# Kernel tuning notes

Hardware: AMD Instinct MI355X
Metric: run time of the kernel (lower is better)

Reference implementation:

```python
import jax, jax.numpy as jnp
import numpy as np

OUTDIM, INPUTDIM, DEGREE = 64, 512, 8


def setup_inputs() -> dict:
    key = jax.random.key(0)
    k1, k2 = jax.random.split(key)
    x = jax.random.normal(k1, (16, 4096, INPUTDIM), dtype=jnp.float32)
    # torch.randn(outdim, inputdim, degree) / (sqrt(inputdim)*sqrt(degree))
    coeffs = jax.random.normal(k2, (OUTDIM, INPUTDIM, DEGREE), dtype=jnp.float32)
    coeffs = coeffs / (np.sqrt(INPUTDIM) * np.sqrt(DEGREE))
    bias = jnp.zeros((1, OUTDIM), dtype=jnp.float32)
    return {"x": x, "coeffs": coeffs, "bias": bias}


def _legendre_basis(xn, degree):
    # Iterative (memoized) Legendre recurrence; xn in [-1, 1], shape [N, I].
    Ps = [jnp.ones_like(xn)]
    if degree > 1:
        Ps.append(xn)
    for n in range(2, degree):
        Ps.append(((2.0 * n - 1.0) * xn * Ps[-1] - (n - 1.0) * Ps[-2]) / n)
    return jnp.stack(Ps, axis=-1)  # [N, I, D]


def reference(x, coeffs, bias):
    outdim, inputdim, degree = coeffs.shape
    outshape = x.shape[:-1] + (outdim,)
    x2 = x.reshape(-1, inputdim)                      # [N, I]
    xmin, xmax = x2.min(), x2.max()                   # global min-max normalize
    xn = 2.0 * (x2 - xmin) / (xmax - xmin) - 1.0
    P = _legendre_basis(xn, degree)                   # [N, I, D]
    y = jnp.einsum("nid,oid->no", P, coeffs)          # contract input & degree
    y = y + bias                                      # [N, O]
    return y.reshape(outshape)
```

## Files before the change

kernel.cpp:

```cpp
#include <hip/hip_runtime.h>
#include <math.h>


typedef __bf16 bf16x8 __attribute__((ext_vector_type(8)));
typedef float f32x4 __attribute__((ext_vector_type(4)));

__global__ __launch_bounds__(256) void k_minmax_partial(
    const float4* __restrict__ x4, int n4, float* __restrict__ pmn, float* __restrict__ pmx)
{
  float mn = 3.4e38f, mx = -3.4e38f;
  int stride = gridDim.x * 256;
  for (int i = blockIdx.x * 256 + threadIdx.x; i < n4; i += stride) {
    float4 v = x4[i];
    mn = fminf(mn, fminf(fminf(v.x, v.y), fminf(v.z, v.w)));
    mx = fmaxf(mx, fmaxf(fmaxf(v.x, v.y), fmaxf(v.z, v.w)));
  }
  #pragma unroll
  for (int off = 32; off > 0; off >>= 1) {
    mn = fminf(mn, __shfl_down(mn, off));
    mx = fmaxf(mx, __shfl_down(mx, off));
  }
  __shared__ float smn[4], smx[4];
  int w = threadIdx.x >> 6;
  if ((threadIdx.x & 63) == 0) { smn[w] = mn; smx[w] = mx; }
  __syncthreads();
  if (threadIdx.x == 0) {
    pmn[blockIdx.x] = fminf(fminf(smn[0], smn[1]), fminf(smn[2], smn[3]));
    pmx[blockIdx.x] = fmaxf(fmaxf(smx[0], smx[1]), fmaxf(smx[2], smx[3]));
  }
}

__global__ __launch_bounds__(256) void k_prep_final(
    const float* __restrict__ coeffs, bf16x8* __restrict__ Bws,
    const float* __restrict__ pmn, const float* __restrict__ pmx, int nb,
    float* __restrict__ so, float* __restrict__ y, const float* __restrict__ bias,
    int doB)
{
  int b = blockIdx.x;
  if (b < 128) {
    if (!doB) return;
    int t = b * 256 + threadIdx.x;
    int lane = t & 63;
    int tile = t >> 6;
    int ct = tile & 3;
    int kt = tile >> 2;
    int i = kt * 4 + (lane >> 4);
    int o = ct * 16 + (lane & 15);
    const float4* cp = (const float4*)(coeffs + ((size_t)o * 512 + i) * 8);
    float4 c0 = cp[0], c1 = cp[1];
    bf16x8 v;
    v[0] = (__bf16)(c0.x);
    v[1] = (__bf16)(c0.y);
    v[2] = (__bf16)(c0.z * 1.5f);
    v[3] = (__bf16)(c0.w * 2.5f);
    v[4] = (__bf16)(c1.x * 4.375f);
    v[5] = (__bf16)(c1.y * 7.875f);
    v[6] = (__bf16)(c1.z * 14.4375f);
    v[7] = (__bf16)(c1.w * 26.8125f);
    Bws[(size_t)(kt * 4 + ct) * 64 + lane] = v;
  } else if (b == 128) {
    float mn = 3.4e38f, mx = -3.4e38f;
    for (int i = threadIdx.x; i < nb; i += 256) {
      mn = fminf(mn, pmn[i]);
      mx = fmaxf(mx, pmx[i]);
    }
    #pragma unroll
    for (int off = 32; off > 0; off >>= 1) {
      mn = fminf(mn, __shfl_down(mn, off));
      mx = fmaxf(mx, __shfl_down(mx, off));
    }
    __shared__ float smn[4], smx[4];
    int w = threadIdx.x >> 6;
    if ((threadIdx.x & 63) == 0) { smn[w] = mn; smx[w] = mx; }
    __syncthreads();
    if (threadIdx.x == 0) {
      mn = fminf(fminf(smn[0], smn[1]), fminf(smn[2], smn[3]));
      mx = fmaxf(fmaxf(smx[0], smx[1]), fmaxf(smx[2], smx[3]));
      float r = mx - mn;
      so[0] = 2.0f / r;
      so[1] = -2.0f * mn / r - 1.0f;
    }
  } else {
    int base = (b - 129) * 1024;
    const float4* b4 = (const float4*)bias;
    float4* y4 = (float4*)y;
    #pragma unroll
    for (int r = 0; r < 4; ++r) {
      int j = base + r * 256 + threadIdx.x;
      y4[j] = b4[j & 15];
    }
  }
}

__global__ __launch_bounds__(256, 4) void k_main(
    const float* __restrict__ x, const bf16x8* __restrict__ Bws,
    const float* __restrict__ so, float* __restrict__ y)
{
  __shared__ __align__(16) float4 smem[2048];

  const float s = so[0], off = so[1];
  const int t    = threadIdx.x;
  const int lane = t & 63;
  const int w    = t >> 6;
  const int m    = lane & 15;
  const int quad = lane >> 4;
  const int bx   = blockIdx.x;
  const int qK   = bx & 3;
  const size_t rowbase = ((size_t)(bx >> 2)) * 128 + (size_t)w * 32;
  const int kb0 = qK * 32;

  const float* xq0 = x + (rowbase +      m) * 512 + (size_t)kb0 * 4 + quad;
  const float* xq1 = x + (rowbase + 16 + m) * 512 + (size_t)kb0 * 4 + quad;

  const float4* bsrc = (const float4*)((const char*)Bws + (size_t)kb0 * 4096);

  f32x4 acc[2][4];
  #pragma unroll
  for (int f = 0; f < 2; ++f)
    #pragma unroll
    for (int ct = 0; ct < 4; ++ct) acc[f][ct] = (f32x4){0.f, 0.f, 0.f, 0.f};

  const float C2 = 0.33333334f, C3 = 0.26666668f, C4 = 0.25714287f;
  const float C5 = 0.25396827f, C6 = 0.25252524f, C7 = 0.25174826f;

  float xr[4][2];
  xr[0][0] = xq0[0];  xr[0][1] = xq1[0];
  xr[1][0] = xq0[4];  xr[1][1] = xq1[4];

  const bf16x8* bw = (const bf16x8*)smem;

  for (int wi = 0; wi < 4; ++wi) {
    __syncthreads();
    {
      const float4* g = bsrc + (size_t)wi * 2048;
      float4 a0 = g[t], a1 = g[t + 256], a2 = g[t + 512], a3 = g[t + 768];
      smem[t] = a0; smem[t + 256] = a1; smem[t + 512] = a2; smem[t + 768] = a3;
      float4 b0 = g[t + 1024], b1 = g[t + 1280], b2 = g[t + 1536], b3 = g[t + 1792];
      smem[t + 1024] = b0; smem[t + 1280] = b1; smem[t + 1536] = b2; smem[t + 1792] = b3;
    }
    __syncthreads();

    bf16x8 Bq[2][4];
    #pragma unroll
    for (int ct = 0; ct < 4; ++ct) Bq[0][ct] = bw[ct * 64 + lane];

    #pragma unroll
    for (int kl = 0; kl < 8; ++kl) {
      const int l = wi * 8 + kl;

      if (kl < 7) {
        #pragma unroll
        for (int ct = 0; ct < 4; ++ct)
          Bq[(kl + 1) & 1][ct] = bw[((kl + 1) * 4 + ct) * 64 + lane];
      }
      {
        const int lp = (l + 2 < 32) ? (l + 2) : 31;
        xr[(kl + 2) & 3][0] = xq0[lp * 4];
        xr[(kl + 2) & 3][1] = xq1[lp * 4];
      }

      bf16x8 a[2];
      #pragma unroll
      for (int f = 0; f < 2; ++f) {
        float xn = fmaf(xr[kl & 3][f], s, off);
        float s2 = fmaf(xn, xn, -C2);
        float s3 = (s2 - C3) * xn;
        float s4 = fmaf(xn, s3, -(C4 * s2));
        float s5 = fmaf(xn, s4, -(C5 * s3));
        float s6 = fmaf(xn, s5, -(C6 * s4));
        float s7 = fmaf(xn, s6, -(C7 * s5));
        bf16x8 av;
        av[0] = (__bf16)1.0f; av[1] = (__bf16)xn; av[2] = (__bf16)s2; av[3] = (__bf16)s3;
        av[4] = (__bf16)s4;   av[5] = (__bf16)s5; av[6] = (__bf16)s6; av[7] = (__bf16)s7;
        a[f] = av;
      }

      #pragma unroll
      for (int f = 0; f < 2; ++f)
        #pragma unroll
        for (int ct = 0; ct < 4; ++ct)
          acc[f][ct] = __builtin_amdgcn_mfma_f32_16x16x32_bf16(a[f], Bq[kl & 1][ct], acc[f][ct], 0, 0, 0);
    }
  }

  #pragma unroll
  for (int f = 0; f < 2; ++f) {
    float* yp = y + (rowbase + f * 16 + quad * 4) * 64 + m;
    #pragma unroll
    for (int ct = 0; ct < 4; ++ct)
      #pragma unroll
      for (int r = 0; r < 4; ++r)
        atomicAdd(yp + r * 64 + ct * 16, acc[f][ct][r]);
  }
}

__global__ __launch_bounds__(256) void k_main_simple(
    const float* __restrict__ x, const float* __restrict__ coeffs,
    const float* __restrict__ bias, const float* __restrict__ so, float* __restrict__ y)
{
  const float s = so[0], off = so[1];
  const int lane = threadIdx.x & 63;
  const int w    = threadIdx.x >> 6;
  const int m    = lane & 15;
  const int quad = lane >> 4;
  const int rowA = blockIdx.x * 64 + w * 16 + m;
  const float* xp = x + (size_t)rowA * 512 + quad;

  f32x4 acc0 = {0.f,0.f,0.f,0.f}, acc1 = acc0, acc2 = acc0, acc3 = acc0;
  const float c3a = 5.f/3.f, c3b = 2.f/3.f, c6a = 11.f/6.f, c6b = 5.f/6.f, c7a = 13.f/7.f, c7b = 6.f/7.f;

  for (int kt = 0; kt < 128; ++kt) {
    float xv = xp[kt * 4];
    int i = kt * 4 + quad;
    bf16x8 b[4];
    #pragma unroll
    for (int ct = 0; ct < 4; ++ct) {
      const float* cp = coeffs + ((size_t)(ct * 16 + m) * 512 + i) * 8;
      #pragma unroll
      for (int j = 0; j < 8; ++j) b[ct][j] = (__bf16)cp[j];
    }
    float xn = fmaf(xv, s, off);
    float p2 = fmaf(1.5f * xn, xn, -0.5f);
    float p3 = fmaf(c3a * xn, p2, -(c3b * xn));
    float p4 = fmaf(1.75f * xn, p3, -(0.75f * p2));
    float p5 = fmaf(1.8f * xn, p4, -(0.8f * p3));
    float p6 = fmaf(c6a * xn, p5, -(c6b * p4));
    float p7 = fmaf(c7a * xn, p6, -(c7b * p5));
    bf16x8 a;
    a[0] = (__bf16)1.0f; a[1] = (__bf16)xn; a[2] = (__bf16)p2; a[3] = (__bf16)p3;
    a[4] = (__bf16)p4;   a[5] = (__bf16)p5; a[6] = (__bf16)p6; a[7] = (__bf16)p7;
    acc0 = __builtin_amdgcn_mfma_f32_16x16x32_bf16(a, b[0], acc0, 0, 0, 0);
    acc1 = __builtin_amdgcn_mfma_f32_16x16x32_bf16(a, b[1], acc1, 0, 0, 0);
    acc2 = __builtin_amdgcn_mfma_f32_16x16x32_bf16(a, b[2], acc2, 0, 0, 0);
    acc3 = __builtin_amdgcn_mfma_f32_16x16x32_bf16(a, b[3], acc3, 0, 0, 0);
  }
  float b0v = bias[m], b1v = bias[16+m], b2v = bias[32+m], b3v = bias[48+m];
  float* yp = y + ((size_t)(blockIdx.x * 64 + w * 16 + quad * 4)) * 64 + m;
  #pragma unroll
  for (int r = 0; r < 4; ++r) {
    yp[r*64+ 0] = acc0[r] + b0v;
    yp[r*64+16] = acc1[r] + b1v;
    yp[r*64+32] = acc2[r] + b2v;
    yp[r*64+48] = acc3[r] + b3v;
  }
}

extern "C" void kernel_launch(void* const* d_in, const int* in_sizes, int n_in,
                              void* d_out, int out_size, void* d_ws, size_t ws_size,
                              hipStream_t stream)
{
  const float* x      = (const float*)d_in[0];
  const float* coeffs = (const float*)d_in[1];
  const float* bias   = (const float*)d_in[2];
  float* y = (float*)d_out;

  long nx = (long)in_sizes[0];
  int  N  = (int)(nx / 512);
  int  n4 = (int)(nx / 4);

  float*  so  = (float*)d_ws;
  float*  pmn = (float*)d_ws + 16;
  float*  pmx = pmn + 4096;
  bf16x8* Bws = (bf16x8*)((char*)d_ws + 65536);

  bool pre = ws_size >= (size_t)(65536 + 4096 * 64 * 2 + 4096);

  const int MMB = 4096;
  k_minmax_partial<<<MMB, 256, 0, stream>>>((const float4*)x, n4, pmn, pmx);
  k_prep_final<<<1153, 256, 0, stream>>>(coeffs, Bws, pmn, pmx, MMB, so, y, bias, pre ? 1 : 0);

  if (pre) {
    k_main<<<(N / 128) * 4, 256, 0, stream>>>(x, Bws, so, y);
  } else {
    k_main_simple<<<N / 64, 256, 0, stream>>>(x, coeffs, bias, so, y);
  }
}
```

Measured before the change: 284.3 us.

## Stage coalesced x tiles and Legendre basis in LDS with register-prefetched pipeline

Each thread now loads contiguous float4 chunks of x instead of strided scalar loads, and evaluates the Legendre basis once per element. The bf16 basis vectors go into a padded LDS buffer (stride 17) that the MFMA fragments then read. B and x for the next slice are prefetched into registers while the current slice is multiplied. The goal is to remove uncoalesced global reads of x and redundant basis work. The cost is more LDS (about 50KB), occupancy lowered to 3 blocks per CU, and an extra barrier per iteration.

After: 266.7 us. -6.2%, faster.

```diff
diff --git a/kernel.cpp b/kernel.cpp
--- a/kernel.cpp
+++ b/kernel.cpp
@@ -4,6 +4,8 @@
 
 typedef __bf16 bf16x8 __attribute__((ext_vector_type(8)));
 typedef float f32x4 __attribute__((ext_vector_type(4)));
+
+#define ASTRIDE 17
 
 __global__ __launch_bounds__(256) void k_minmax_partial(
     const float4* __restrict__ x4, int n4, float* __restrict__ pmn, float* __restrict__ pmx)
@@ -92,11 +94,14 @@
   }
 }
 
-__global__ __launch_bounds__(256, 4) void k_main(
+__global__ __launch_bounds__(256, 3) void k_main(
     const float* __restrict__ x, const bf16x8* __restrict__ Bws,
     const float* __restrict__ so, float* __restrict__ y)
 {
-  __shared__ __align__(16) float4 smem[2048];
+  __shared__ __align__(16) char smem[51200];
+  bf16x8* As = (bf16x8*)smem;
+  bf16x8* Bs = (bf16x8*)(smem + 34816);
+  float4* Bs4 = (float4*)Bs;
 
   const float s = so[0], off = so[1];
   const int t    = threadIdx.x;
@@ -106,13 +111,18 @@
   const int quad = lane >> 4;
   const int bx   = blockIdx.x;
   const int qK   = bx & 3;
-  const size_t rowbase = ((size_t)(bx >> 2)) * 128 + (size_t)w * 32;
-  const int kb0 = qK * 32;
-
-  const float* xq0 = x + (rowbase +      m) * 512 + (size_t)kb0 * 4 + quad;
-  const float* xq1 = x + (rowbase + 16 + m) * 512 + (size_t)kb0 * 4 + quad;
-
-  const float4* bsrc = (const float4*)((const char*)Bws + (size_t)kb0 * 4096);
+  const size_t rowbase = ((size_t)(bx >> 2)) * 128;
+
+  const int srow  = t >> 1;
+  const int shalf = t & 1;
+  const float* xg = x + (rowbase + srow) * 512 + qK * 128 + shalf * 8;
+  const int awbase = srow * ASTRIDE + shalf * 8;
+
+  const float4* bsrc = (const float4*)(Bws + (size_t)qK * 32 * 256);
+
+  int arb[2];
+  #pragma unroll
+  for (int f = 0; f < 2; ++f) arb[f] = (w * 32 + f * 16 + m) * ASTRIDE + quad;
 
   f32x4 acc[2][4];
   #pragma unroll
@@ -123,69 +133,63 @@
   const float C2 = 0.33333334f, C3 = 0.26666668f, C4 = 0.25714287f;
   const float C5 = 0.25396827f, C6 = 0.25252524f, C7 = 0.25174826f;
 
-  float xr[4][2];
-  xr[0][0] = xq0[0];  xr[0][1] = xq1[0];
-  xr[1][0] = xq0[4];  xr[1][1] = xq1[4];
-
-  const bf16x8* bw = (const bf16x8*)smem;
-
-  for (int wi = 0; wi < 4; ++wi) {
+  float4 xv0 = *(const float4*)(xg);
+  float4 xv1 = *(const float4*)(xg + 4);
+  float4 bv0 = bsrc[t], bv1 = bsrc[t + 256], bv2 = bsrc[t + 512], bv3 = bsrc[t + 768];
+
+  for (int wi = 0; wi < 8; ++wi) {
+    float xe[8] = {xv0.x, xv0.y, xv0.z, xv0.w, xv1.x, xv1.y, xv1.z, xv1.w};
+    #pragma unroll
+    for (int e = 0; e < 8; ++e) {
+      float xn = fmaf(xe[e], s, off);
+      float s2 = fmaf(xn, xn, -C2);
+      float s3 = (s2 - C3) * xn;
+      float s4 = fmaf(xn, s3, -(C4 * s2));
+      float s5 = fmaf(xn, s4, -(C5 * s3));
+      float s6 = fmaf(xn, s5, -(C6 * s4));
+      float s7 = fmaf(xn, s6, -(C7 * s5));
+      bf16x8 av;
+      av[0] = (__bf16)1.0f; av[1] = (__bf16)xn; av[2] = (__bf16)s2; av[3] = (__bf16)s3;
+      av[4] = (__bf16)s4;   av[5] = (__bf16)s5; av[6] = (__bf16)s6; av[7] = (__bf16)s7;
+      As[awbase + e] = av;
+    }
+    Bs4[t] = bv0; Bs4[t + 256] = bv1; Bs4[t + 512] = bv2; Bs4[t + 768] = bv3;
     __syncthreads();
-    {
-      const float4* g = bsrc + (size_t)wi * 2048;
-      float4 a0 = g[t], a1 = g[t + 256], a2 = g[t + 512], a3 = g[t + 768];
-      smem[t] = a0; smem[t + 256] = a1; smem[t + 512] = a2; smem[t + 768] = a3;
-      float4 b0 = g[t + 1024], b1 = g[t + 1280], b2 = g[t + 1536], b3 = g[t + 1792];
-      smem[t + 1024] = b0; smem[t + 1280] = b1; smem[t + 1536] = b2; smem[t + 1792] = b3;
-    }
-    __syncthreads();
-
-    bf16x8 Bq[2][4];
-    #pragma unroll
-    for (int ct = 0; ct < 4; ++ct) Bq[0][ct] = bw[ct * 64 + lane];
-
-    #pragma unroll
-    for (int kl = 0; kl < 8; ++kl) {
-      const int l = wi * 8 + kl;
-
-      if (kl < 7) {
+
+    if (wi < 7) {
+      const float* xgn = xg + (wi + 1) * 16;
+      xv0 = *(const float4*)(xgn);
+      xv1 = *(const float4*)(xgn + 4);
+      const float4* bn = bsrc + (size_t)(wi + 1) * 1024;
+      bv0 = bn[t]; bv1 = bn[t + 256]; bv2 = bn[t + 512]; bv3 = bn[t + 768];
+    }
+
+    bf16x8 Aq[2][2], Bq[2][4];
+    #pragma unroll
+    for (int f = 0; f < 2; ++f) Aq[0][f] = As[arb[f]];
+    #pragma unroll
+    for (int ct = 0; ct < 4; ++ct) Bq[0][ct] = Bs[ct * 64 + lane];
+
+    #pragma unroll
+    for (int ktl = 0; ktl < 4; ++ktl) {
+      if (ktl < 3) {
         #pragma unroll
-        for (int ct = 0; ct < 4; ++ct)
-          Bq[(kl + 1) & 1][ct] = bw[((kl + 1) * 4 + ct) * 64 + lane];
+        for (int f = 0; f < 2; ++f) Aq[(ktl + 1) & 1][f] = As[arb[f] + (ktl + 1) * 4];
+        #pragma unroll
+        for (int ct = 0; ct < 4; ++ct) Bq[(ktl + 1) & 1][ct] = Bs[((ktl + 1) * 4 + ct) * 64 + lane];
       }
-      {
-        const int lp = (l + 2 < 32) ? (l + 2) : 31;
-        xr[(kl + 2) & 3][0] = xq0[lp * 4];
-        xr[(kl + 2) & 3][1] = xq1[lp * 4];
-      }
-
-      bf16x8 a[2];
-      #pragma unroll
-      for (int f = 0; f < 2; ++f) {
-        float xn = fmaf(xr[kl & 3][f], s, off);
-        float s2 = fmaf(xn, xn, -C2);
-        float s3 = (s2 - C3) * xn;
-        float s4 = fmaf(xn, s3, -(C4 * s2));
-        float s5 = fmaf(xn, s4, -(C5 * s3));
-        float s6 = fmaf(xn, s5, -(C6 * s4));
-        float s7 = fmaf(xn, s6, -(C7 * s5));
-        bf16x8 av;
-        av[0] = (__bf16)1.0f; av[1] = (__bf16)xn; av[2] = (__bf16)s2; av[3] = (__bf16)s3;
-        av[4] = (__bf16)s4;   av[5] = (__bf16)s5; av[6] = (__bf16)s6; av[7] = (__bf16)s7;
-        a[f] = av;
-      }
-
       #pragma unroll
       for (int f = 0; f < 2; ++f)
         #pragma unroll
         for (int ct = 0; ct < 4; ++ct)
-          acc[f][ct] = __builtin_amdgcn_mfma_f32_16x16x32_bf16(a[f], Bq[kl & 1][ct], acc[f][ct], 0, 0, 0);
-    }
+          acc[f][ct] = __builtin_amdgcn_mfma_f32_16x16x32_bf16(Aq[ktl & 1][f], Bq[ktl & 1][ct], acc[f][ct], 0, 0, 0);
+    }
+    __syncthreads();
   }
 
   #pragma unroll
   for (int f = 0; f < 2; ++f) {
-    float* yp = y + (rowbase + f * 16 + quad * 4) * 64 + m;
+    float* yp = y + (rowbase + w * 32 + f * 16 + quad * 4) * 64 + m;
     #pragma unroll
     for (int ct = 0; ct < 4; ++ct)
       #pragma unroll
```
